# Kernel tuning notes

Measured on AMD Instinct MI355X. Metric: run time of the kernel, lower is better.

Reference implementation:

```python
import math
import jax, jax.numpy as jnp
import numpy as np

B, C_IN, H, W = 32, 96, 64, 64
OUT = 128
EXC = int(OUT * 0.8)   # 102 excitatory channels
INH = OUT - EXC        # 26 inhibitory channels
K = 5
PAD = 2                # kernel//2 so all stages keep spatial size


def _sm_kernel(kernel_size=5, sigma_e=1.2, sigma_i=1.4):
    c = kernel_size // 2
    xx, yy = np.meshgrid(np.arange(kernel_size), np.arange(kernel_size), indexing='ij')
    xx = xx.astype(np.float32) - c
    yy = yy.astype(np.float32) - c
    ge = np.exp(-(xx ** 2 + yy ** 2) / (2 * sigma_e ** 2))
    gi = np.exp(-(xx ** 2 + yy ** 2) / (2 * sigma_i ** 2))
    dog = ge / (2 * math.pi * sigma_e ** 2) - gi / (2 * math.pi * sigma_i ** 2)
    dog = dog / dog[c, c]
    return jnp.asarray(dog[None, None], dtype=jnp.float32)  # [1,1,K,K]


def setup_inputs() -> dict:
    key = jax.random.key(0)
    k1, k2, k3, k4 = jax.random.split(key, 4)
    wr = 25.0 / math.sqrt(C_IN * K * K)
    x = jax.random.normal(k1, (B, C_IN, H, W), jnp.float32)
    w_ee = wr * jnp.abs(jax.random.normal(k2, (EXC, C_IN, K, K), jnp.float32))
    w_ei = wr * jnp.abs(jax.random.normal(k3, (INH, EXC, K, K), jnp.float32))
    w_ie = -wr * jnp.abs(jax.random.normal(k4, (EXC, INH, K, K), jnp.float32))
    return {"x": x, "w_ee": w_ee, "w_ei": w_ei, "w_ie": w_ie, "sm_kernel": _sm_kernel()}


def _reflect_pad(x, p):
    if p == 0:
        return x
    return jnp.pad(x, ((0, 0), (0, 0), (p, p), (p, p)), mode='reflect')


def _conv(x, w, pad=0, groups=1):
    return jax.lax.conv_general_dilated(
        x, w, window_strides=(1, 1), padding=[(pad, pad), (pad, pad)],
        dimension_numbers=('NCHW', 'OIHW', 'NCHW'), feature_group_count=groups)


def _forward(x, w_ee, w_ei, w_ie, sm_kernel):
    y_e = _conv(_reflect_pad(x, PAD), w_ee)                 # [B,EXC,H,W], act=Identity
    y_i = jax.nn.relu(_conv(_reflect_pad(y_e, PAD), w_ei))  # [B,INH,H,W]
    y_ie = _conv(_reflect_pad(y_i, PAD), w_ie)              # [B,EXC,H,W]
    y = y_e + y_ie
    # depthwise surround-modulation conv (zero padding, as in F.conv2d)
    w_sm = jnp.tile(sm_kernel, (EXC, 1, 1, 1))              # [EXC,1,K,K]
    y = _conv(y, w_sm, pad=K // 2, groups=EXC)
    return y, y_e, y_i


def reference(x, w_ee, w_ei, w_ie, sm_kernel):
    y, y_e, y_i = _forward(x, w_ee, w_ei, w_ie, sm_kernel)

    # --- hard WTA masks (winner channel per (b,h,w) position) ---
    win_e = jnp.argmax(y_e, axis=1)                                        # [B,H,W]
    mask_e = (jnp.arange(EXC)[None, :, None, None] == win_e[:, None]).astype(y_e.dtype)
    y_wta_e = y_e * mask_e
    win_i = jnp.argmax(jnp.abs(y_i), axis=1)
    mask_i = (jnp.arange(INH)[None, :, None, None] == win_i[:, None]).astype(y_i.dtype)
    y_wta_i = y_i * mask_i

    # --- transpose-conv outer-product trick; with same-size feature maps the
    # conv collapses to a 1x1 full correlation over (b,h,w) -> einsum ---
    yx_ee = jnp.einsum('bchw,behw->ec', x, y_wta_e)[:, :, None, None]      # [EXC,C_IN,1,1]
    yx_ei = jnp.einsum('behw,bihw->ie', y_wta_e, y_wta_i)[:, :, None, None]  # [INH,EXC,1,1]
    yx_ie = jnp.einsum('bihw,behw->ei', y_wta_i, y)[:, :, None, None]      # [EXC,INH,1,1]

    yu_e = jnp.sum(y_wta_e, axis=(0, 2, 3))[:, None, None, None]           # [EXC,1,1,1]
    yu_i = jnp.sum(jnp.abs(y_wta_i), axis=(0, 2, 3))[:, None, None, None]  # [INH,1,1,1]

    upd_ee = yx_ee - yu_e * w_ee   # broadcasts to [EXC,C_IN,K,K]
    upd_ei = yx_ei - yu_i * w_ei
    upd_ie = yx_ie - yu_e * w_ie
    upd_ee = upd_ee / (jnp.abs(upd_ee).max() + 1e-8)
    upd_ei = upd_ei / (jnp.abs(upd_ei).max() + 1e-8)
    upd_ie = upd_ie / (jnp.abs(upd_ie).max() + 1e-8)

    return (y, upd_ee, upd_ei, upd_ie)
```

## Files before the change

kernel.cpp:

```cpp
#include <hip/hip_runtime.h>

#define B_    32
#define CIN_  96
#define EXC_  102
#define INH_  26
#define HH    64
#define WW    64
#define HW_   4096
#define NPOS  (B_*HW_)
#define EEPAD 97

typedef short bf8 __attribute__((ext_vector_type(8)));
typedef float f32x4 __attribute__((ext_vector_type(4)));

__device__ __forceinline__ int refl(int i) {
    if (i < 0) i = -i;
    if (i > 63) i = 126 - i;
    return i;
}

__device__ __forceinline__ short f2bf(float f) {
    unsigned u = __float_as_uint(f);
    return (short)((u + 0x7fffu + ((u >> 16) & 1u)) >> 16);
}

template<int C, int CPAD>
__global__ __launch_bounds__(256) void pack_nhwc(
    const float* __restrict__ src, short* __restrict__ dst)
{
    const int b = blockIdx.z;
    const int pos = blockIdx.x*64 + (threadIdx.x & 63);
    const int cg0 = threadIdx.x >> 6;
    for (int cg = cg0; cg < CPAD/8; cg += 4) {
        bf8 v;
#pragma unroll
        for (int j = 0; j < 8; ++j) {
            int c = cg*8 + j;
            float f = (c < C) ? src[((size_t)b*C + c)*HW_ + pos] : 0.f;
            v[j] = f2bf(f);
        }
        *(bf8*)(&dst[((size_t)b*HW_ + pos)*CPAD + cg*8]) = v;
    }
}

template<int N, int C, int NPAD, int CPAD>
__global__ void pack_w(const float* __restrict__ src, short* __restrict__ dst)
{
    int idx = blockIdx.x*256 + threadIdx.x;
    if (idx >= 25*NPAD*CPAD) return;
    int tap = idx / (NPAD*CPAD);
    int rem = idx - tap*NPAD*CPAD;
    int n = rem / CPAD, c = rem - n*CPAD;
    float f = (n < N && c < C) ? src[((size_t)n*C + c)*25 + tap] : 0.f;
    dst[idx] = f2bf(f);
}

template<int CPAD, int NPAD, int NT, int COUT, int NCHUNK, bool RELU, bool ADDIN>
__global__ __launch_bounds__(256, 2) void conv_mfma(
    const short* __restrict__ src, const short* __restrict__ wgt,
    const float* __restrict__ addin, float* __restrict__ out)
{
    __shared__ __align__(16) short sA[400*40];
    const int t  = threadIdx.x;
    const int bx = blockIdx.x;
    const int b  = blockIdx.z;
    const int h0 = (bx >> 2) * 16;
    const int w0 = (bx &  3) * 16;
    const int lane = t & 63;
    const int wv = t >> 6;
    const int nh = lane & 15;
    const int q  = lane >> 4;

    int goff[7], loff[7];
#pragma unroll
    for (int s = 0; s < 7; ++s) {
        int i = t + 256*s;
        if (i < 1600) {
            int rec = i >> 2, seg = i & 3;
            int lh = rec / 20, lw = rec - lh*20;
            int gh = refl(h0 - 2 + lh), gw = refl(w0 - 2 + lw);
            goff[s] = (b*HW_ + gh*WW + gw) * CPAD + seg*8;
            loff[s] = rec*40 + seg*8;
        } else { goff[s] = 0; loff[s] = -1; }
    }

    f32x4 acc[4][NT];
#pragma unroll
    for (int mt = 0; mt < 4; ++mt)
#pragma unroll
        for (int nt = 0; nt < NT; ++nt) {
            f32x4 z = {0.f, 0.f, 0.f, 0.f};
            acc[mt][nt] = z;
        }

    int abase[4];
#pragma unroll
    for (int mt = 0; mt < 4; ++mt)
        abase[mt] = ((wv*4 + mt)*20 + nh)*40 + q*8;

    for (int ck = 0; ck < NCHUNK; ++ck) {
        const int c0 = ck*32;
        __syncthreads();
#pragma unroll
        for (int s = 0; s < 7; ++s)
            if (loff[s] >= 0)
                *(bf8*)(&sA[loff[s]]) = *(const bf8*)(&src[goff[s] + c0]);
        __syncthreads();
        const short* wch = wgt + c0 + nh*CPAD + q*8;
        for (int dh = 0; dh < 5; ++dh) {
#pragma unroll
            for (int dw = 0; dw < 5; ++dw) {
                const int tap = dh*5 + dw;
                bf8 bfr[NT];
#pragma unroll
                for (int nt = 0; nt < NT; ++nt)
                    bfr[nt] = *(const bf8*)(&wch[(size_t)(tap*NPAD + nt*16)*CPAD]);
                bf8 afr[4];
#pragma unroll
                for (int mt = 0; mt < 4; ++mt)
                    afr[mt] = *(const bf8*)(&sA[abase[mt] + (dh*20 + dw)*40]);
#pragma unroll
                for (int mt = 0; mt < 4; ++mt)
#pragma unroll
                    for (int nt = 0; nt < NT; ++nt)
                        acc[mt][nt] = __builtin_amdgcn_mfma_f32_16x16x32_bf16(
                            afr[mt], bfr[nt], acc[mt][nt], 0, 0, 0);
            }
        }
    }

#pragma unroll
    for (int mt = 0; mt < 4; ++mt) {
        const int rowi = h0 + wv*4 + mt;
#pragma unroll
        for (int nt = 0; nt < NT; ++nt) {
            const int chn = nt*16 + nh;
            if (chn < COUT) {
                size_t obase = ((size_t)(b*COUT + chn))*HW_ + rowi*WW + w0 + q*4;
#pragma unroll
                for (int r = 0; r < 4; ++r) {
                    float v = acc[mt][nt][r];
                    if (RELU) v = fmaxf(v, 0.f);
                    if (ADDIN) v += addin[obase + r];
                    out[obase + r] = v;
                }
            }
        }
    }
}

__global__ __launch_bounds__(256) void smconv_v2(
    const float* __restrict__ in, const float* __restrict__ sm,
    float* __restrict__ out)
{
    __shared__ __align__(16) float sx[36*36];
    const int tid = threadIdx.x;
    const int tile = blockIdx.x;
    const int e = blockIdx.y;
    const int b = blockIdx.z;
    const int h0 = (tile >> 1) * 32, w0 = (tile & 1) * 32;
    const int r  = tid >> 3;
    const int cg = (tid & 7) * 4;
    const float* inc = in + ((size_t)(b*EXC_ + e))*HW_;
#pragma unroll
    for (int it = 0; it < 6; ++it) {
        int i = tid + it*256;
        if (i < 1296) {
            int lh = i / 36, lw = i - lh*36;
            int gh = h0 - 2 + lh, gw = w0 - 2 + lw;
            float v = 0.f;
            if (gh >= 0 && gh < HH && gw >= 0 && gw < WW) v = inc[gh*WW + gw];
            sx[i] = v;
        }
    }
    __syncthreads();
    float a0 = 0.f, a1 = 0.f, a2 = 0.f, a3 = 0.f;
#pragma unroll
    for (int kh = 0; kh < 5; ++kh) {
        const float4* rowp = (const float4*)(sx + (r + kh)*36 + cg);
        float4 v0 = rowp[0], v1 = rowp[1];
        float xv[8] = {v0.x, v0.y, v0.z, v0.w, v1.x, v1.y, v1.z, v1.w};
#pragma unroll
        for (int kw = 0; kw < 5; ++kw) {
            float wv = sm[kh*5 + kw];
            a0 = fmaf(xv[kw+0], wv, a0);
            a1 = fmaf(xv[kw+1], wv, a1);
            a2 = fmaf(xv[kw+2], wv, a2);
            a3 = fmaf(xv[kw+3], wv, a3);
        }
    }
    size_t oidx = ((size_t)(b*EXC_ + e))*HW_ + (h0 + r)*WW + w0 + cg;
    *(float4*)(out + oidx) = make_float4(a0, a1, a2, a3);
}

__global__ void wta_kernel(const float* __restrict__ in, int* __restrict__ win,
                           float* __restrict__ val, int C, int use_abs)
{
    int p = blockIdx.x*256 + threadIdx.x;
    int b = p >> 12, hw = p & 4095;
    const float* base = in + ((size_t)b*C)*HW_ + hw;
    float bestv = base[0];
    float bestk = use_abs ? fabsf(bestv) : bestv;
    int besti = 0;
    for (int c = 1; c < C; ++c) {
        float v = base[(size_t)c*HW_];
        float key = use_abs ? fabsf(v) : v;
        if (key > bestk) { bestk = key; bestv = v; besti = c; }
    }
    win[p] = besti;
    val[p] = bestv;
}

__global__ __launch_bounds__(256) void scatter_ee_kernel(
    const float* __restrict__ x, const int* __restrict__ win_e,
    const float* __restrict__ val_e, float* __restrict__ yx_ee,
    float* __restrict__ yu_e)
{
    __shared__ float s_yx[EXC_*EEPAD];
    __shared__ float s_yu[EXC_];
    for (int i = threadIdx.x; i < EXC_*EEPAD; i += 256) s_yx[i] = 0.f;
    if (threadIdx.x < EXC_) s_yu[threadIdx.x] = 0.f;
    __syncthreads();
    int p = blockIdx.x * 256 + threadIdx.x;
    int b = p >> 12, hw = p & 4095;
    int wi = win_e[p]; float v = val_e[p];
    atomicAdd(&s_yu[wi], v);
    const float* xb = x + ((size_t)b*CIN_)*HW_ + hw;
    float* row = s_yx + wi*EEPAD;
    for (int c = 0; c < CIN_; ++c)
        atomicAdd(&row[c], v * xb[(size_t)c*HW_]);
    __syncthreads();
    for (int i = threadIdx.x; i < EXC_*CIN_; i += 256) {
        int e = i / CIN_, c = i - e*CIN_;
        float vv = s_yx[e*EEPAD + c];
        if (vv != 0.f) atomicAdd(&yx_ee[i], vv);
    }
    if (threadIdx.x < EXC_) {
        float vv = s_yu[threadIdx.x];
        if (vv != 0.f) atomicAdd(&yu_e[threadIdx.x], vv);
    }
}

__global__ __launch_bounds__(256) void scatter_ei_kernel(
    const int* __restrict__ win_e, const float* __restrict__ val_e,
    const int* __restrict__ win_i, const float* __restrict__ val_i,
    float* __restrict__ yx_ei, float* __restrict__ yu_i)
{
    __shared__ float s[INH_*EXC_ + INH_];
    for (int i = threadIdx.x; i < INH_*EXC_ + INH_; i += 256) s[i] = 0.f;
    __syncthreads();
    int p = blockIdx.x * 256 + threadIdx.x;
    int we = win_e[p]; float ve = val_e[p];
    int wi = win_i[p]; float vi = val_i[p];
    atomicAdd(&s[wi*EXC_ + we], ve*vi);
    atomicAdd(&s[INH_*EXC_ + wi], fabsf(vi));
    __syncthreads();
    for (int i = threadIdx.x; i < INH_*EXC_ + INH_; i += 256) {
        float v = s[i];
        if (v != 0.f) {
            if (i < INH_*EXC_) atomicAdd(&yx_ei[i], v);
            else               atomicAdd(&yu_i[i - INH_*EXC_], v);
        }
    }
}

__global__ __launch_bounds__(256) void scatter_ie_kernel(
    const float* __restrict__ y, const int* __restrict__ win_i,
    const float* __restrict__ val_i, float* __restrict__ yx_ie)
{
    __shared__ float s[EXC_*INH_];
    for (int i = threadIdx.x; i < EXC_*INH_; i += 256) s[i] = 0.f;
    __syncthreads();
    int p = blockIdx.x * 256 + threadIdx.x;
    int b = p >> 12, hw = p & 4095;
    int wi = win_i[p]; float v = val_i[p];
    if (v != 0.f) {
        const float* yb = y + ((size_t)b*EXC_)*HW_ + hw;
        for (int e = 0; e < EXC_; ++e)
            atomicAdd(&s[e*INH_ + wi], v * yb[(size_t)e*HW_]);
    }
    __syncthreads();
    for (int i = threadIdx.x; i < EXC_*INH_; i += 256) {
        float v = s[i];
        if (v != 0.f) atomicAdd(&yx_ie[i], v);
    }
}

__global__ void upd_absmax_kernel(const float* __restrict__ yx,
    const float* __restrict__ yu, const float* __restrict__ w,
    int E, int C, unsigned int* __restrict__ amax)
{
    __shared__ unsigned int sm_;
    if (threadIdx.x == 0) sm_ = 0u;
    __syncthreads();
    int n = E*C*25;
    float m = 0.f;
    for (int idx = blockIdx.x*256 + threadIdx.x; idx < n; idx += gridDim.x*256) {
        int ec = idx / 25;
        int e = ec / C;
        float v = yx[ec] - yu[e]*w[idx];
        m = fmaxf(m, fabsf(v));
    }
    atomicMax(&sm_, __float_as_uint(m));
    __syncthreads();
    if (threadIdx.x == 0) atomicMax(amax, sm_);
}

__global__ void upd_write_kernel(const float* __restrict__ yx,
    const float* __restrict__ yu, const float* __restrict__ w,
    int E, int C, const unsigned int* __restrict__ amax,
    float* __restrict__ out)
{
    int n = E*C*25;
    int idx = blockIdx.x*256 + threadIdx.x;
    if (idx >= n) return;
    int ec = idx / 25;
    int e = ec / C;
    float v = yx[ec] - yu[e]*w[idx];
    float mx = __uint_as_float(*amax);
    out[idx] = v / (mx + 1e-8f);
}

extern "C" void kernel_launch(void* const* d_in, const int* in_sizes, int n_in,
                              void* d_out, int out_size, void* d_ws, size_t ws_size,
                              hipStream_t stream)
{
    const float* x    = (const float*)d_in[0];
    const float* w_ee = (const float*)d_in[1];
    const float* w_ei = (const float*)d_in[2];
    const float* w_ie = (const float*)d_in[3];
    const float* smk  = (const float*)d_in[4];
    float* out = (float*)d_out;

    float* y_e = (float*)d_ws;
    float* y_i = y_e + (size_t)B_*EXC_*HW_;
    short* R   = (short*)(y_i + (size_t)B_*INH_*HW_);
    short* wee = R + (size_t)16777216;
    short* wei = wee + 268800;
    short* wie = wei + 102400;
    int*   win_e = (int*)(wie + 89600);
    float* val_e = (float*)(win_e + NPOS);
    int*   win_i = (int*)(val_e + NPOS);
    float* val_i = (float*)(win_i + NPOS);
    float* yx_ee = val_i + NPOS;
    float* yx_ei = yx_ee + EXC_*CIN_;
    float* yx_ie = yx_ei + INH_*EXC_;
    float* yu_e  = yx_ie + EXC_*INH_;
    float* yu_i  = yu_e + EXC_;
    unsigned int* amax = (unsigned int*)(yu_i + INH_);

    hipMemsetAsync(yx_ee, 0,
        (size_t)(EXC_*CIN_ + INH_*EXC_ + EXC_*INH_ + EXC_ + INH_ + 3)*sizeof(float),
        stream);

    pack_w<EXC_, CIN_, 112, 96><<<(25*112*96 + 255)/256, 256, 0, stream>>>(w_ee, wee);
    pack_w<INH_, EXC_, 32, 128><<<(25*32*128 + 255)/256, 256, 0, stream>>>(w_ei, wei);
    pack_w<EXC_, INH_, 112, 32><<<(25*112*32 + 255)/256, 256, 0, stream>>>(w_ie, wie);
    pack_nhwc<CIN_, 96><<<dim3(64, 1, B_), 256, 0, stream>>>(x, R);

    conv_mfma<96, 112, 7, EXC_, 3, false, false>
        <<<dim3(16, 1, B_), 256, 0, stream>>>(R, wee, nullptr, y_e);
    wta_kernel<<<NPOS/256, 256, 0, stream>>>(y_e, win_e, val_e, EXC_, 0);

    pack_nhwc<EXC_, 128><<<dim3(64, 1, B_), 256, 0, stream>>>(y_e, R);
    conv_mfma<128, 32, 2, INH_, 4, true, false>
        <<<dim3(16, 1, B_), 256, 0, stream>>>(R, wei, nullptr, y_i);
    wta_kernel<<<NPOS/256, 256, 0, stream>>>(y_i, win_i, val_i, INH_, 1);

    pack_nhwc<INH_, 32><<<dim3(64, 1, B_), 256, 0, stream>>>(y_i, R);
    conv_mfma<32, 112, 7, EXC_, 1, false, true>
        <<<dim3(16, 1, B_), 256, 0, stream>>>(R, wie, y_e, y_e);

    smconv_v2<<<dim3(4, EXC_, B_), 256, 0, stream>>>(y_e, smk, out);

    scatter_ee_kernel<<<512, 256, 0, stream>>>(x, win_e, val_e, yx_ee, yu_e);
    scatter_ei_kernel<<<512, 256, 0, stream>>>(win_e, val_e, win_i, val_i, yx_ei, yu_i);
    scatter_ie_kernel<<<512, 256, 0, stream>>>(out, win_i, val_i, yx_ie);

    upd_absmax_kernel<<<240, 256, 0, stream>>>(yx_ee, yu_e, w_ee, EXC_, CIN_, amax+0);
    upd_absmax_kernel<<<240, 256, 0, stream>>>(yx_ei, yu_i, w_ei, INH_, EXC_, amax+1);
    upd_absmax_kernel<<<240, 256, 0, stream>>>(yx_ie, yu_e, w_ie, EXC_, INH_, amax+2);

    float* out_ee = out + (size_t)B_*EXC_*HW_;
    float* out_ei = out_ee + EXC_*CIN_*25;
    float* out_ie = out_ei + INH_*EXC_*25;
    upd_write_kernel<<<(EXC_*CIN_*25+255)/256, 256, 0, stream>>>(yx_ee, yu_e, w_ee, EXC_, CIN_, amax+0, out_ee);
    upd_write_kernel<<<(INH_*EXC_*25+255)/256, 256, 0, stream>>>(yx_ei, yu_i, w_ei, INH_, EXC_, amax+1, out_ei);
    upd_write_kernel<<<(EXC_*INH_*25+255)/256, 256, 0, stream>>>(yx_ie, yu_e, w_ie, EXC_, INH_, amax+2, out_ie);
}
```

Measured before the change: 604.9 us.

## Prefetch conv taps, replace global atomics with partial reductions, fuse small kernels

The conv inner loop now double-buffers the A and B fragments, loading the next tap while MFMAs run on the current one. The ee and ie scatter kernels write per-block partial sums to a workspace instead of issuing global atomics, and a separate reduce kernel sums those partials. The three weight-pack, three absmax and three update-write launches are each merged into a single launch. The combined changes target launch overhead and global atomic contention, at the cost of extra workspace traffic and higher register pressure in the conv.

```diff
diff --git a/kernel.cpp b/kernel.cpp
--- a/kernel.cpp
+++ b/kernel.cpp
@@ -9,6 +9,12 @@
 #define HW_   4096
 #define NPOS  (B_*HW_)
 #define EEPAD 97
+#define NPART 512
+#define NEE   (EXC_*CIN_ + EXC_)
+#define NIE   (EXC_*INH_)
+#define N1U   (EXC_*CIN_*25)
+#define N2U   (INH_*EXC_*25)
+#define N3U   (EXC_*INH_*25)
 
 typedef short bf8 __attribute__((ext_vector_type(8)));
 typedef float f32x4 __attribute__((ext_vector_type(4)));
@@ -43,16 +49,21 @@
     }
 }
 
-template<int N, int C, int NPAD, int CPAD>
-__global__ void pack_w(const float* __restrict__ src, short* __restrict__ dst)
-{
-    int idx = blockIdx.x*256 + threadIdx.x;
-    if (idx >= 25*NPAD*CPAD) return;
+__global__ __launch_bounds__(256) void pack_w3(
+    const float* __restrict__ w_ee, const float* __restrict__ w_ei,
+    const float* __restrict__ w_ie, short* __restrict__ dst)
+{
+    int gi = blockIdx.x*256 + threadIdx.x;
+    if (gi >= 460800) return;
+    const float* src; int N, C, NPAD, CPAD; int idx;
+    if (gi < 268800)      { src = w_ee; N = 102; C = 96;  NPAD = 112; CPAD = 96;  idx = gi; }
+    else if (gi < 371200) { src = w_ei; N = 26;  C = 102; NPAD = 32;  CPAD = 128; idx = gi - 268800; }
+    else                  { src = w_ie; N = 102; C = 26;  NPAD = 112; CPAD = 32;  idx = gi - 371200; }
     int tap = idx / (NPAD*CPAD);
-    int rem = idx - tap*NPAD*CPAD;
+    int rem = idx - tap*(NPAD*CPAD);
     int n = rem / CPAD, c = rem - n*CPAD;
     float f = (n < N && c < C) ? src[((size_t)n*C + c)*25 + tap] : 0.f;
-    dst[idx] = f2bf(f);
+    dst[gi] = f2bf(f);
 }
 
 template<int CPAD, int NPAD, int NT, int COUT, int NCHUNK, bool RELU, bool ADDIN>
@@ -107,25 +118,30 @@
                 *(bf8*)(&sA[loff[s]]) = *(const bf8*)(&src[goff[s] + c0]);
         __syncthreads();
         const short* wch = wgt + c0 + nh*CPAD + q*8;
-        for (int dh = 0; dh < 5; ++dh) {
-#pragma unroll
-            for (int dw = 0; dw < 5; ++dw) {
-                const int tap = dh*5 + dw;
-                bf8 bfr[NT];
+
+        bf8 bfr[2][NT];
+        bf8 afr[2][4];
+        auto LOADTAP = [&](int buf, int tap_) {
+            const int dh_ = tap_ / 5, dw_ = tap_ - 5*dh_;
+#pragma unroll
+            for (int nt = 0; nt < NT; ++nt)
+                bfr[buf][nt] = *(const bf8*)(&wch[(size_t)(tap_*NPAD + nt*16)*CPAD]);
+#pragma unroll
+            for (int mt = 0; mt < 4; ++mt)
+                afr[buf][mt] = *(const bf8*)(&sA[abase[mt] + (dh_*20 + dw_)*40]);
+        };
+
+        LOADTAP(0, 0);
+#pragma unroll
+        for (int tap = 0; tap < 25; ++tap) {
+            const int cur = tap & 1;
+            if (tap < 24) LOADTAP(cur ^ 1, tap + 1);
+#pragma unroll
+            for (int mt = 0; mt < 4; ++mt)
 #pragma unroll
                 for (int nt = 0; nt < NT; ++nt)
-                    bfr[nt] = *(const bf8*)(&wch[(size_t)(tap*NPAD + nt*16)*CPAD]);
-                bf8 afr[4];
-#pragma unroll
-                for (int mt = 0; mt < 4; ++mt)
-                    afr[mt] = *(const bf8*)(&sA[abase[mt] + (dh*20 + dw)*40]);
-#pragma unroll
-                for (int mt = 0; mt < 4; ++mt)
-#pragma unroll
-                    for (int nt = 0; nt < NT; ++nt)
-                        acc[mt][nt] = __builtin_amdgcn_mfma_f32_16x16x32_bf16(
-                            afr[mt], bfr[nt], acc[mt][nt], 0, 0, 0);
-            }
+                    acc[mt][nt] = __builtin_amdgcn_mfma_f32_16x16x32_bf16(
+                        afr[cur][mt], bfr[cur][nt], acc[mt][nt], 0, 0, 0);
         }
     }
 
@@ -213,8 +229,7 @@
 
 __global__ __launch_bounds__(256) void scatter_ee_kernel(
     const float* __restrict__ x, const int* __restrict__ win_e,
-    const float* __restrict__ val_e, float* __restrict__ yx_ee,
-    float* __restrict__ yu_e)
+    const float* __restrict__ val_e, float* __restrict__ parts)
 {
     __shared__ float s_yx[EXC_*EEPAD];
     __shared__ float s_yu[EXC_];
@@ -230,15 +245,12 @@
     for (int c = 0; c < CIN_; ++c)
         atomicAdd(&row[c], v * xb[(size_t)c*HW_]);
     __syncthreads();
+    float* dst = parts + (size_t)blockIdx.x * NEE;
     for (int i = threadIdx.x; i < EXC_*CIN_; i += 256) {
         int e = i / CIN_, c = i - e*CIN_;
-        float vv = s_yx[e*EEPAD + c];
-        if (vv != 0.f) atomicAdd(&yx_ee[i], vv);
-    }
-    if (threadIdx.x < EXC_) {
-        float vv = s_yu[threadIdx.x];
-        if (vv != 0.f) atomicAdd(&yu_e[threadIdx.x], vv);
-    }
+        dst[i] = s_yx[e*EEPAD + c];
+    }
+    if (threadIdx.x < EXC_) dst[EXC_*CIN_ + threadIdx.x] = s_yu[threadIdx.x];
 }
 
 __global__ __launch_bounds__(256) void scatter_ei_kernel(
@@ -266,7 +278,7 @@
 
 __global__ __launch_bounds__(256) void scatter_ie_kernel(
     const float* __restrict__ y, const int* __restrict__ win_i,
-    const float* __restrict__ val_i, float* __restrict__ yx_ie)
+    const float* __restrict__ val_i, float* __restrict__ parts)
 {
     __shared__ float s[EXC_*INH_];
     for (int i = threadIdx.x; i < EXC_*INH_; i += 256) s[i] = 0.f;
@@ -280,45 +292,88 @@
             atomicAdd(&s[e*INH_ + wi], v * yb[(size_t)e*HW_]);
     }
     __syncthreads();
-    for (int i = threadIdx.x; i < EXC_*INH_; i += 256) {
-        float v = s[i];
-        if (v != 0.f) atomicAdd(&yx_ie[i], v);
-    }
-}
-
-__global__ void upd_absmax_kernel(const float* __restrict__ yx,
-    const float* __restrict__ yu, const float* __restrict__ w,
-    int E, int C, unsigned int* __restrict__ amax)
-{
-    __shared__ unsigned int sm_;
-    if (threadIdx.x == 0) sm_ = 0u;
-    __syncthreads();
-    int n = E*C*25;
-    float m = 0.f;
-    for (int idx = blockIdx.x*256 + threadIdx.x; idx < n; idx += gridDim.x*256) {
-        int ec = idx / 25;
-        int e = ec / C;
-        float v = yx[ec] - yu[e]*w[idx];
-        m = fmaxf(m, fabsf(v));
-    }
-    atomicMax(&sm_, __float_as_uint(m));
-    __syncthreads();
-    if (threadIdx.x == 0) atomicMax(amax, sm_);
-}
-
-__global__ void upd_write_kernel(const float* __restrict__ yx,
-    const float* __restrict__ yu, const float* __restrict__ w,
-    int E, int C, const unsigned int* __restrict__ amax,
-    float* __restrict__ out)
-{
-    int n = E*C*25;
+    float* dst = parts + (size_t)blockIdx.x * NIE;
+    for (int i = threadIdx.x; i < EXC_*INH_; i += 256) dst[i] = s[i];
+}
+
+__global__ __launch_bounds__(256) void reduce_parts_kernel(
+    const float* __restrict__ parts, float* __restrict__ dst, int n)
+{
+    __shared__ float s[256];
+    int i = blockIdx.x*64 + (threadIdx.x & 63);
+    int g = threadIdx.x >> 6;
+    float a = 0.f;
+    if (i < n) {
+        for (int j = g*128; j < g*128 + 128; ++j)
+            a += parts[(size_t)j*n + i];
+    }
+    s[threadIdx.x] = a;
+    __syncthreads();
+    if (threadIdx.x < 64 && i < n)
+        dst[i] = s[threadIdx.x] + s[threadIdx.x+64] + s[threadIdx.x+128] + s[threadIdx.x+192];
+}
+
+__global__ __launch_bounds__(256) void upd_absmax3(
+    const float* __restrict__ yx_ee, const float* __restrict__ yu_e,
+    const float* __restrict__ w_ee,
+    const float* __restrict__ yx_ei, const float* __restrict__ yu_i,
+    const float* __restrict__ w_ei,
+    const float* __restrict__ yx_ie, const float* __restrict__ w_ie,
+    unsigned int* __restrict__ amax)
+{
+    float m0 = 0.f, m1 = 0.f, m2 = 0.f;
+    for (int idx = blockIdx.x*256 + threadIdx.x; idx < N1U + N2U + N3U;
+         idx += gridDim.x*256) {
+        if (idx < N1U) {
+            int ec = idx / 25; int e = ec / CIN_;
+            m0 = fmaxf(m0, fabsf(yx_ee[ec] - yu_e[e]*w_ee[idx]));
+        } else if (idx < N1U + N2U) {
+            int j = idx - N1U; int ec = j / 25; int e = ec / EXC_;
+            m1 = fmaxf(m1, fabsf(yx_ei[ec] - yu_i[e]*w_ei[j]));
+        } else {
+            int j = idx - N1U - N2U; int ec = j / 25; int e = ec / INH_;
+            m2 = fmaxf(m2, fabsf(yx_ie[ec] - yu_e[e]*w_ie[j]));
+        }
+    }
+    __shared__ unsigned int s0, s1, s2;
+    if (threadIdx.x == 0) { s0 = 0u; s1 = 0u; s2 = 0u; }
+    __syncthreads();
+    atomicMax(&s0, __float_as_uint(m0));
+    atomicMax(&s1, __float_as_uint(m1));
+    atomicMax(&s2, __float_as_uint(m2));
+    __syncthreads();
+    if (threadIdx.x == 0) {
+        atomicMax(&amax[0], s0);
+        atomicMax(&amax[1], s1);
+        atomicMax(&amax[2], s2);
+    }
+}
+
+__global__ __launch_bounds__(256) void upd_write3(
+    const float* __restrict__ yx_ee, const float* __restrict__ yu_e,
+    const float* __restrict__ w_ee,
+    const float* __restrict__ yx_ei, const float* __restrict__ yu_i,
+    const float* __restrict__ w_ei,
+    const float* __restrict__ yx_ie, const float* __restrict__ w_ie,
+    const unsigned int* __restrict__ amax,
+    float* __restrict__ out_ee, float* __restrict__ out_ei,
+    float* __restrict__ out_ie)
+{
     int idx = blockIdx.x*256 + threadIdx.x;
-    if (idx >= n) return;
-    int ec = idx / 25;
-    int e = ec / C;
-    float v = yx[ec] - yu[e]*w[idx];
-    float mx = __uint_as_float(*amax);
-    out[idx] = v / (mx + 1e-8f);
+    if (idx >= N1U + N2U + N3U) return;
+    if (idx < N1U) {
+        int ec = idx / 25; int e = ec / CIN_;
+        float v = yx_ee[ec] - yu_e[e]*w_ee[idx];
+        out_ee[idx] = v / (__uint_as_float(amax[0]) + 1e-8f);
+    } else if (idx < N1U + N2U) {
+        int j = idx - N1U; int ec = j / 25; int e = ec / EXC_;
+        float v = yx_ei[ec] - yu_i[e]*w_ei[j];
+        out_ei[j] = v / (__uint_as_float(amax[1]) + 1e-8f);
+    } else {
+        int j = idx - N1U - N2U; int ec = j / 25; int e = ec / INH_;
+        float v = yx_ie[ec] - yu_e[e]*w_ie[j];
+        out_ie[j] = v / (__uint_as_float(amax[2]) + 1e-8f);
+    }
 }
 
 extern "C" void kernel_launch(void* const* d_in, const int* in_sizes, int n_in,
@@ -343,19 +398,17 @@
     int*   win_i = (int*)(val_e + NPOS);
     float* val_i = (float*)(win_i + NPOS);
     float* yx_ee = val_i + NPOS;
-    float* yx_ei = yx_ee + EXC_*CIN_;
-    float* yx_ie = yx_ei + INH_*EXC_;
-    float* yu_e  = yx_ie + EXC_*INH_;
-    float* yu_i  = yu_e + EXC_;
+    float* yu_e  = yx_ee + EXC_*CIN_;
+    float* yx_ie = yu_e + EXC_;
+    float* yx_ei = yx_ie + EXC_*INH_;
+    float* yu_i  = yx_ei + INH_*EXC_;
     unsigned int* amax = (unsigned int*)(yu_i + INH_);
-
-    hipMemsetAsync(yx_ee, 0,
-        (size_t)(EXC_*CIN_ + INH_*EXC_ + EXC_*INH_ + EXC_ + INH_ + 3)*sizeof(float),
-        stream);
-
-    pack_w<EXC_, CIN_, 112, 96><<<(25*112*96 + 255)/256, 256, 0, stream>>>(w_ee, wee);
-    pack_w<INH_, EXC_, 32, 128><<<(25*32*128 + 255)/256, 256, 0, stream>>>(w_ei, wei);
-    pack_w<EXC_, INH_, 112, 32><<<(25*112*32 + 255)/256, 256, 0, stream>>>(w_ie, wie);
+    float* parts_ee = (float*)R;
+    float* parts_ie = parts_ee + (size_t)NPART*NEE;
+
+    hipMemsetAsync(yx_ei, 0, (size_t)(INH_*EXC_ + INH_ + 3)*sizeof(float), stream);
+
+    pack_w3<<<1800, 256, 0, stream>>>(w_ee, w_ei, w_ie, wee);
     pack_nhwc<CIN_, 96><<<dim3(64, 1, B_), 256, 0, stream>>>(x, R);
 
     conv_mfma<96, 112, 7, EXC_, 3, false, false>
@@ -373,18 +426,18 @@
 
     smconv_v2<<<dim3(4, EXC_, B_), 256, 0, stream>>>(y_e, smk, out);
 
-    scatter_ee_kernel<<<512, 256, 0, stream>>>(x, win_e, val_e, yx_ee, yu_e);
-    scatter_ei_kernel<<<512, 256, 0, stream>>>(win_e, val_e, win_i, val_i, yx_ei, yu_i);
-    scatter_ie_kernel<<<512, 256, 0, stream>>>(out, win_i, val_i, yx_ie);
-
-    upd_absmax_kernel<<<240, 256, 0, stream>>>(yx_ee, yu_e, w_ee, EXC_, CIN_, amax+0);
-    upd_absmax_kernel<<<240, 256, 0, stream>>>(yx_ei, yu_i, w_ei, INH_, EXC_, amax+1);
-    upd_absmax_kernel<<<240, 256, 0, stream>>>(yx_ie, yu_e, w_ie, EXC_, INH_, amax+2);
-
+    scatter_ee_kernel<<<NPART, 256, 0, stream>>>(x, win_e, val_e, parts_ee);
+    scatter_ei_kernel<<<NPART, 256, 0, stream>>>(win_e, val_e, win_i, val_i, yx_ei, yu_i);
+    scatter_ie_kernel<<<NPART, 256, 0, stream>>>(out, win_i, val_i, parts_ie);
+    reduce_parts_kernel<<<(NEE + 63)/64, 256, 0, stream>>>(parts_ee, yx_ee, NEE);
+    reduce_parts_kernel<<<(NIE + 63)/64, 256, 0, stream>>>(parts_ie, yx_ie, NIE);
+
+    upd_absmax3<<<480, 256, 0, stream>>>(yx_ee, yu_e, w_ee, yx_ei, yu_i, w_ei,
+                                         yx_ie, w_ie, amax);
     float* out_ee = out + (size_t)B_*EXC_*HW_;
-    float* out_ei = out_ee + EXC_*CIN_*25;
-    float* out_ie = out_ei + INH_*EXC_*25;
-    upd_write_kernel<<<(EXC_*CIN_*25+255)/256, 256, 0, stream>>>(yx_ee, yu_e, w_ee, EXC_, CIN_, amax+0, out_ee);
-    upd_write_kernel<<<(INH_*EXC_*25+255)/256, 256, 0, stream>>>(yx_ei, yu_i, w_ei, INH_, EXC_, amax+1, out_ei);
-    upd_write_kernel<<<(EXC_*INH_*25+255)/256, 256, 0, stream>>>(yx_ie, yu_e, w_ie, EXC_, INH_, amax+2, out_ie);
-}
+    float* out_ei = out_ee + N1U;
+    float* out_ie = out_ei + N2U;
+    upd_write3<<<(N1U + N2U + N3U + 255)/256, 256, 0, stream>>>(
+        yx_ee, yu_e, w_ee, yx_ei, yu_i, w_ei, yx_ie, w_ie, amax,
+        out_ee, out_ei, out_ie);
+}
```

Measured after the change: 638.0 us. +5.5%, slower.
